# Kernel tuning notes

Measured on AMD Instinct MI355X. Metric: run time of the kernel, lower is better.

Reference implementation:

```python
import jax, jax.numpy as jnp
import numpy as np

H = 12          # num heads
D = 768         # hidden size
DH = D // H     # head dim = 64
DE = 768        # encoder hidden size


def setup_inputs() -> dict:
    key = jax.random.key(0)
    ks = jax.random.split(key, 10)
    s = 0.02
    return {
        "hidden_states": jax.random.normal(ks[0], (2, 2048, D), dtype=jnp.float32),
        "encoder_hidden_states": jax.random.normal(ks[1], (2, 4096, DE), dtype=jnp.float32),
        "Wq": jax.random.normal(ks[2], (D, D), dtype=jnp.float32) * s,
        "bq": jnp.zeros((D,), dtype=jnp.float32),
        "Wk": jax.random.normal(ks[3], (DE, D), dtype=jnp.float32) * s,
        "bk": jnp.zeros((D,), dtype=jnp.float32),
        "Wv": jax.random.normal(ks[4], (DE, D), dtype=jnp.float32) * s,
        "bv": jnp.zeros((D,), dtype=jnp.float32),
        "Wo": jax.random.normal(ks[5], (D, D), dtype=jnp.float32) * s,
        "bo": jnp.zeros((D,), dtype=jnp.float32),
    }


def _split_heads(x):
    # [B, S, D] -> [B, H, S, DH]
    B, S, _ = x.shape
    return x.reshape(B, S, H, DH).transpose(0, 2, 1, 3)


def reference(hidden_states, encoder_hidden_states, Wq, bq, Wk, bk, Wv, bv, Wo, bo):
    q = _split_heads(hidden_states @ Wq + bq)              # [B,H,Sq,DH]
    k = _split_heads(encoder_hidden_states @ Wk + bk)      # [B,H,Skv,DH]
    v = _split_heads(encoder_hidden_states @ Wv + bv)      # [B,H,Skv,DH]
    scale = 1.0 / jnp.sqrt(jnp.asarray(DH, dtype=q.dtype))
    scores = jnp.einsum("bhqd,bhkd->bhqk", q, k) * scale   # [B,H,Sq,Skv]
    probs = jax.nn.softmax(scores, axis=-1)
    ctx = jnp.einsum("bhqk,bhkd->bhqd", probs, v)          # [B,H,Sq,DH]
    B, _, Sq, _ = ctx.shape
    ctx = ctx.transpose(0, 2, 1, 3).reshape(B, Sq, D)      # [B,Sq,D]
    return ctx @ Wo + bo
```

## Files before the change

### kernel.cpp

```cpp
#include <hip/hip_runtime.h>

typedef __attribute__((ext_vector_type(8))) short bf16x8;
typedef __attribute__((ext_vector_type(4))) float f32x4;
typedef __attribute__((ext_vector_type(8))) unsigned short u16x8;
typedef __attribute__((ext_vector_type(4))) unsigned short u16x4;
typedef __attribute__((ext_vector_type(4))) int i32x4;

static constexpr int Bsz = 2, SQ = 2048, SKV = 4096, Dm = 768, NH = 12, DH = 64;

#define WAITV(N) asm volatile("s_waitcnt vmcnt(" #N ")" ::: "memory")
#define WAITL0() asm volatile("s_waitcnt lgkmcnt(0)" ::: "memory")

static __device__ __forceinline__ unsigned short f2bf(float f) {
  unsigned int u = __float_as_uint(f);
  u += 0x7fff + ((u >> 16) & 1);
  return (unsigned short)(u >> 16);
}

static __device__ __forceinline__ float fexp2(float x) {
#if __has_builtin(__builtin_amdgcn_exp2f)
  return __builtin_amdgcn_exp2f(x);
#else
  float r; asm("v_exp_f32 %0, %1" : "=v"(r) : "v"(x)); return r;
#endif
}

static __device__ __forceinline__ int cvtpk(float lo, float hi) {
  int r; asm("v_cvt_pk_bf16_f32 %0, %1, %2" : "=v"(r) : "v"(lo), "v"(hi));
  return r;
}

__global__ void cvt2_kernel(const float* __restrict__ a, const float* __restrict__ b,
                            unsigned short* __restrict__ out, int n1, int ntot) {
  int i = blockIdx.x * blockDim.x + threadIdx.x;
  if (i >= ntot) return;
  const float4* p = (i < n1) ? (reinterpret_cast<const float4*>(a) + (size_t)i * 2)
                             : (reinterpret_cast<const float4*>(b) + (size_t)(i - n1) * 2);
  float4 x = p[0], y = p[1];
  u16x8 o;
  o[0] = f2bf(x.x); o[1] = f2bf(x.y); o[2] = f2bf(x.z); o[3] = f2bf(x.w);
  o[4] = f2bf(y.x); o[5] = f2bf(y.y); o[6] = f2bf(y.z); o[7] = f2bf(y.w);
  *(reinterpret_cast<u16x8*>(out) + i) = o;
}

__global__ void wtrans4(const float* __restrict__ Wq, const float* __restrict__ Wk,
                        const float* __restrict__ Wv, const float* __restrict__ Wo,
                        unsigned short* __restrict__ oq, unsigned short* __restrict__ ok,
                        unsigned short* __restrict__ ov, unsigned short* __restrict__ oo) {
  __shared__ float t[32][33];
  const int z = blockIdx.z;
  const float* W = (z == 0) ? Wq : (z == 1) ? Wk : (z == 2) ? Wv : Wo;
  unsigned short* WT = (z == 0) ? oq : (z == 1) ? ok : (z == 2) ? ov : oo;
  int n0 = blockIdx.x * 32, k0 = blockIdx.y * 32;
  int tx = threadIdx.x, ty = threadIdx.y;
  #pragma unroll
  for (int i = 0; i < 4; ++i)
    t[ty * 4 + i][tx] = W[(size_t)(k0 + ty * 4 + i) * Dm + n0 + tx];
  __syncthreads();
  #pragma unroll
  for (int i = 0; i < 4; ++i)
    WT[(size_t)(n0 + ty * 4 + i) * Dm + k0 + tx] = f2bf(t[tx][ty * 4 + i]);
}

__global__ void vtrans(const unsigned short* __restrict__ vb, unsigned short* __restrict__ vtp) {
  __shared__ unsigned short t[64][65];
  const int kt = blockIdx.x, h = blockIdx.y, b = blockIdx.z;
  const int tid = threadIdx.x;
  const int kr = tid >> 2, dc = (tid & 3) * 16;
  const unsigned short* src = vb + ((size_t)(b * SKV + kt * 64 + kr)) * Dm + h * DH + dc;
  u16x8 a0 = *(const u16x8*)src, a1 = *(const u16x8*)(src + 8);
  #pragma unroll
  for (int j = 0; j < 8; ++j) { t[kr][dc + j] = a0[j]; t[kr][dc + 8 + j] = a1[j]; }
  __syncthreads();
  const int d = tid >> 2, p0 = (tid & 3) * 16;
  u16x8 o0, o1;
  #pragma unroll
  for (int j = 0; j < 16; ++j) {
    int pos = p0 + j;
    int pos5 = pos & 31;
    int kv5 = ((pos5 >> 3) & 3) * 4 + ((pos5 >> 2) & 1) * 16 + (pos5 & 3);
    int kv = (pos & 32) | kv5;
    unsigned short v = t[kv][d];
    if (j < 8) o0[j] = v; else o1[j - 8] = v;
  }
  unsigned short* dst = vtp + ((size_t)(b * NH + h) * DH + d) * SKV + kt * 64 + p0;
  *(u16x8*)dst = o0;
  *(u16x8*)(dst + 8) = o1;
}

template <int BM, int BN, bool F32OUT>
static __device__ __forceinline__ void gemm_body(const unsigned short* __restrict__ A,
                                                 const unsigned short* __restrict__ BT,
                                                 const float* __restrict__ bias,
                                                 void* __restrict__ Cout, float scale,
                                                 int row0, int col0,
                                                 unsigned short* As, unsigned short* Bs) {
  const int tid = threadIdx.x;
  const int wave = tid >> 6, lane = tid & 63;
  const int wr = wave >> 1, wc = wave & 1;
  const int lrow = lane & 15, lg = lane >> 4, lk8 = lg << 3;
  constexpr int MI = BM / 32, NJ = BN / 32;
  constexpr int AG = BM / 64, BG = BN / 64, LPS = AG + BG;
  constexpr int KS = Dm / 32;
  f32x4 acc[MI][NJ] = {};

  const unsigned short* ap[AG]; int ae[AG];
  const unsigned short* bp[BG]; int be[BG];
  #pragma unroll
  for (int j = 0; j < AG; ++j) {
    int e = (tid + j * 256) * 8; int r = e >> 5, c = e & 31;
    ap[j] = A + (size_t)(row0 + r) * Dm + c; ae[j] = e;
  }
  #pragma unroll
  for (int j = 0; j < BG; ++j) {
    int e = (tid + j * 256) * 8; int r = e >> 5, c = e & 31;
    bp[j] = BT + (size_t)(col0 + r) * Dm + c; be[j] = e;
  }

  auto stage = [&](int buf) {
    #pragma unroll
    for (int j = 0; j < AG; ++j) {
      __builtin_amdgcn_global_load_lds(
          (const __attribute__((address_space(1))) void*)ap[j],
          (__attribute__((address_space(3))) void*)(As + buf * (BM * 32) + ae[j]), 16, 0, 0);
      ap[j] += 32;
    }
    #pragma unroll
    for (int j = 0; j < BG; ++j) {
      __builtin_amdgcn_global_load_lds(
          (const __attribute__((address_space(1))) void*)bp[j],
          (__attribute__((address_space(3))) void*)(Bs + buf * (BN * 32) + be[j]), 16, 0, 0);
      bp[j] += 32;
    }
  };

  auto step = [&](int buf, bool doStage, bool last) {
    if (last) { WAITV(0); }
    else { if constexpr (LPS == 4) { WAITV(4); } else { WAITV(3); } }
    __builtin_amdgcn_s_barrier();
    bf16x8 a[MI], b[NJ];
    #pragma unroll
    for (int mi = 0; mi < MI; ++mi)
      a[mi] = *(const bf16x8*)&As[buf * (BM * 32) + (wr * (BM / 2) + mi * 16 + lrow) * 32 + lk8];
    #pragma unroll
    for (int nj = 0; nj < NJ; ++nj)
      b[nj] = *(const bf16x8*)&Bs[buf * (BN * 32) + (wc * (BN / 2) + nj * 16 + lrow) * 32 + lk8];
    WAITL0();
    __builtin_amdgcn_s_barrier();
    if (doStage) stage(buf);
    #pragma unroll
    for (int mi = 0; mi < MI; ++mi)
      #pragma unroll
      for (int nj = 0; nj < NJ; ++nj)
        acc[mi][nj] = __builtin_amdgcn_mfma_f32_16x16x32_bf16(b[nj], a[mi], acc[mi][nj], 0, 0, 0);
  };

  stage(0); stage(1);
  for (int ki = 0; ki + 2 < KS; ki += 2) { step(0, true, false); step(1, true, false); }
  step(0, false, false);
  step(1, false, true);

  #pragma unroll
  for (int mi = 0; mi < MI; ++mi) {
    const int grow = row0 + wr * (BM / 2) + mi * 16 + lrow;
    #pragma unroll
    for (int nj = 0; nj < NJ; ++nj) {
      const int gcolb = col0 + wc * (BN / 2) + nj * 16 + (lg << 2);
      const f32x4 bb = *(const f32x4*)&bias[gcolb];
      if constexpr (F32OUT) {
        f32x4 v;
        #pragma unroll
        for (int r = 0; r < 4; ++r) v[r] = (acc[mi][nj][r] + bb[r]) * scale;
        *(f32x4*)((float*)Cout + (size_t)grow * Dm + gcolb) = v;
      } else {
        u16x4 o;
        #pragma unroll
        for (int r = 0; r < 4; ++r) o[r] = f2bf((acc[mi][nj][r] + bb[r]) * scale);
        *(u16x4*)((unsigned short*)Cout + (size_t)grow * Dm + gcolb) = o;
      }
    }
  }
}

__global__ __launch_bounds__(256) void qkv_gemm(const unsigned short* __restrict__ hsb,
                                                const unsigned short* __restrict__ ehsb,
                                                const unsigned short* __restrict__ wqt,
                                                const unsigned short* __restrict__ wkt,
                                                const unsigned short* __restrict__ wvt,
                                                const float* __restrict__ bq,
                                                const float* __restrict__ bk,
                                                const float* __restrict__ bv,
                                                unsigned short* __restrict__ qb,
                                                unsigned short* __restrict__ kb,
                                                unsigned short* __restrict__ vb) {
  __shared__ unsigned short As[2 * 128 * 32];
  __shared__ unsigned short Bs[2 * 128 * 32];
  const int tile = blockIdx.y;
  const unsigned short *A, *BT; const float* bias; unsigned short* out;
  float scale; int row0;
  if (tile < 32)      { A = hsb;  BT = wqt; bias = bq; out = qb; scale = 0.18033688f; row0 = tile * 128; }
  else if (tile < 96) { A = ehsb; BT = wkt; bias = bk; out = kb; scale = 1.0f;        row0 = (tile - 32) * 128; }
  else                { A = ehsb; BT = wvt; bias = bv; out = vb; scale = 1.0f;        row0 = (tile - 96) * 128; }
  gemm_body<128, 128, false>(A, BT, bias, out, scale, row0, blockIdx.x * 128, As, Bs);
}

__global__ __launch_bounds__(256) void o_gemm(const unsigned short* __restrict__ A,
                                              const unsigned short* __restrict__ BT,
                                              const float* __restrict__ bias,
                                              float* __restrict__ Cout) {
  __shared__ unsigned short As[2 * 128 * 32];
  __shared__ unsigned short Bs[2 * 64 * 32];
  gemm_body<128, 64, true>(A, BT, bias, Cout, 1.0f, blockIdx.y * 128, blockIdx.x * 64, As, Bs);
}

__global__ __launch_bounds__(256) void attn_kernel(const unsigned short* __restrict__ Q,
                                                   const unsigned short* __restrict__ K,
                                                   const unsigned short* __restrict__ VT,
                                                   unsigned short* __restrict__ Ctx) {
  __shared__ unsigned short Ks[2][64 * 64];
  __shared__ unsigned short Vs[2][64 * 64];
  const int qt = blockIdx.x, h = blockIdx.y, b = blockIdx.z;
  const int tid = threadIdx.x;
  const int wave = tid >> 6, lane = tid & 63;
  const int lrow = lane & 15, lg = lane >> 4, lk8 = lg << 3;
  const size_t qoff = (size_t)b * SQ * Dm + (size_t)h * DH;
  const size_t koff = (size_t)b * SKV * Dm + (size_t)h * DH;
  const size_t voff = (size_t)(b * NH + h) * DH * SKV;

  const int qrow = qt * 64 + wave * 16 + lrow;
  const bf16x8 qa0 = *(const bf16x8*)(Q + qoff + (size_t)qrow * Dm + lk8);
  const bf16x8 qa1 = *(const bf16x8*)(Q + qoff + (size_t)qrow * Dm + 32 + lk8);

  bf16x8 ones;
  #pragma unroll
  for (int j = 0; j < 8; ++j) ones[j] = (short)0x3F80;

  const unsigned short *kp0, *kp1, *vp0, *vp1;
  int de0, de1;
  {
    int db0 = tid * 16, db1 = (tid + 256) * 16;
    int r0 = db0 >> 7, cb0 = db0 & 127, r1 = db1 >> 7, cb1 = db1 & 127;
    int sc0 = (cb0 ^ ((r0 & 7) << 4)) >> 1, sc1 = (cb1 ^ ((r1 & 7) << 4)) >> 1;
    kp0 = K + koff + (size_t)r0 * Dm + sc0;  kp1 = K + koff + (size_t)r1 * Dm + sc1;
    vp0 = VT + voff + (size_t)r0 * SKV + sc0; vp1 = VT + voff + (size_t)r1 * SKV + sc1;
    de0 = db0 >> 1; de1 = db1 >> 1;
  }

  auto stage = [&](int buf) {
    __builtin_amdgcn_global_load_lds((const __attribute__((address_space(1))) void*)kp0,
        (__attribute__((address_space(3))) void*)(&Ks[buf][de0]), 16, 0, 0);
    __builtin_amdgcn_global_load_lds((const __attribute__((address_space(1))) void*)vp0,
        (__attribute__((address_space(3))) void*)(&Vs[buf][de0]), 16, 0, 0);
    __builtin_amdgcn_global_load_lds((const __attribute__((address_space(1))) void*)kp1,
        (__attribute__((address_space(3))) void*)(&Ks[buf][de1]), 16, 0, 0);
    __builtin_amdgcn_global_load_lds((const __attribute__((address_space(1))) void*)vp1,
        (__attribute__((address_space(3))) void*)(&Vs[buf][de1]), 16, 0, 0);
    kp0 += 64 * Dm; kp1 += 64 * Dm; vp0 += 64; vp1 += 64;
  };

  f32x4 acc[4] = {};
  f32x4 acc_l = {};
  const int swz = (lrow & 7) << 4;

  auto tilebody = [&](int buf, bool doStage, bool last) {
    if (last) { WAITV(0); } else { WAITV(4); }
    __builtin_amdgcn_s_barrier();

    f32x4 s[4] = {};
    __builtin_amdgcn_s_setprio(1);
    #pragma unroll
    for (int ks = 0; ks < 2; ++ks)
      #pragma unroll
      for (int nj = 0; nj < 4; ++nj) {
        const int cb = (ks * 64 + lg * 16) ^ swz;
        bf16x8 kf = *(const bf16x8*)((const char*)&Ks[buf][0] + (nj * 16 + lrow) * 128 + cb);
        s[nj] = __builtin_amdgcn_mfma_f32_16x16x32_bf16(kf, ks ? qa1 : qa0, s[nj], 0, 0, 0);
      }
    __builtin_amdgcn_s_setprio(0);

    float e[4][4];
    #pragma unroll
    for (int nj = 0; nj < 4; ++nj)
      #pragma unroll
      for (int r = 0; r < 4; ++r) e[nj][r] = fexp2(s[nj][r]);

    #pragma unroll
    for (int ks = 0; ks < 2; ++ks) {
      i32x4 pw;
      pw[0] = cvtpk(e[2 * ks][0], e[2 * ks][1]);
      pw[1] = cvtpk(e[2 * ks][2], e[2 * ks][3]);
      pw[2] = cvtpk(e[2 * ks + 1][0], e[2 * ks + 1][1]);
      pw[3] = cvtpk(e[2 * ks + 1][2], e[2 * ks + 1][3]);
      bf16x8 pa = __builtin_bit_cast(bf16x8, pw);
      __builtin_amdgcn_s_setprio(1);
      #pragma unroll
      for (int dj = 0; dj < 4; ++dj) {
        const int cb = (ks * 64 + lg * 16) ^ swz;
        bf16x8 vf = *(const bf16x8*)((const char*)&Vs[buf][0] + (dj * 16 + lrow) * 128 + cb);
        acc[dj] = __builtin_amdgcn_mfma_f32_16x16x32_bf16(vf, pa, acc[dj], 0, 0, 0);
      }
      acc_l = __builtin_amdgcn_mfma_f32_16x16x32_bf16(ones, pa, acc_l, 0, 0, 0);
      __builtin_amdgcn_s_setprio(0);
    }

    WAITL0();
    __builtin_amdgcn_s_barrier();
    if (doStage) stage(buf);
  };

  stage(0); stage(1);
  constexpr int NT = SKV / 64;
  for (int t = 0; t + 2 < NT; t += 2) { tilebody(0, true, false); tilebody(1, true, false); }
  tilebody(0, false, false);
  tilebody(1, false, true);

  const float linv = 1.0f / acc_l[0];
  #pragma unroll
  for (int dj = 0; dj < 4; ++dj) {
    u16x4 o;
    #pragma unroll
    for (int r = 0; r < 4; ++r) o[r] = f2bf(acc[dj][r] * linv);
    *(u16x4*)(Ctx + qoff + (size_t)qrow * Dm + dj * 16 + (lg << 2)) = o;
  }
}

extern "C" void kernel_launch(void* const* d_in, const int* in_sizes, int n_in,
                              void* d_out, int out_size, void* d_ws, size_t ws_size,
                              hipStream_t stream) {
  const float* hs  = (const float*)d_in[0];
  const float* ehs = (const float*)d_in[1];
  const float* Wq  = (const float*)d_in[2];
  const float* bq  = (const float*)d_in[3];
  const float* Wk  = (const float*)d_in[4];
  const float* bk  = (const float*)d_in[5];
  const float* Wv  = (const float*)d_in[6];
  const float* bv  = (const float*)d_in[7];
  const float* Wo  = (const float*)d_in[8];
  const float* bo  = (const float*)d_in[9];
  float* out = (float*)d_out;

  unsigned short* hsb  = (unsigned short*)d_ws;
  unsigned short* ehsb = hsb  + (size_t)Bsz * SQ * Dm;
  unsigned short* wqt  = ehsb + (size_t)Bsz * SKV * Dm;
  unsigned short* wkt  = wqt + (size_t)Dm * Dm;
  unsigned short* wvt  = wkt + (size_t)Dm * Dm;
  unsigned short* wot  = wvt + (size_t)Dm * Dm;
  unsigned short* qb   = wot + (size_t)Dm * Dm;
  unsigned short* kb   = qb  + (size_t)Bsz * SQ * Dm;
  unsigned short* vb   = kb  + (size_t)Bsz * SKV * Dm;
  unsigned short* ctxb = vb  + (size_t)Bsz * SKV * Dm;
  unsigned short* vtp  = ehsb;

  const int nHS = Bsz * SQ * Dm, nEHS = Bsz * SKV * Dm;
  const int n1 = nHS / 8, ntot = (nHS + nEHS) / 8;
  cvt2_kernel<<<(ntot + 255) / 256, 256, 0, stream>>>(hs, ehs, hsb, n1, ntot);

  wtrans4<<<dim3(24, 24, 4), dim3(32, 8), 0, stream>>>(Wq, Wk, Wv, Wo, wqt, wkt, wvt, wot);

  qkv_gemm<<<dim3(6, 160), 256, 0, stream>>>(hsb, ehsb, wqt, wkt, wvt, bq, bk, bv, qb, kb, vb);

  vtrans<<<dim3(SKV / 64, NH, Bsz), 256, 0, stream>>>(vb, vtp);

  attn_kernel<<<dim3(SQ / 64, NH, Bsz), 256, 0, stream>>>(qb, kb, vtp, ctxb);

  o_gemm<<<dim3(12, 32), 256, 0, stream>>>(ctxb, wot, bo, out);
}
```

Baseline: 247.8 us.

## Triple-buffer GEMM and attention pipelines, two query strips per attention wave

Both the GEMM body and the attention kernel move from double to triple LDS buffering. The next tile is staged right after a single barrier instead of behind a second barrier and lgkmcnt wait. The attention kernel now runs 128 threads, where each wave covers 32 query rows (two 16-row strips), so every K/V fragment read from LDS feeds twice as many MFMAs. This cuts barriers per iteration and LDS traffic per FLOP, at the cost of more registers per wave and more LDS per block, which may lower occupancy.

```diff
diff --git a/kernel.cpp b/kernel.cpp
--- a/kernel.cpp
+++ b/kernel.cpp
@@ -9,7 +9,7 @@
 static constexpr int Bsz = 2, SQ = 2048, SKV = 4096, Dm = 768, NH = 12, DH = 64;
 
 #define WAITV(N) asm volatile("s_waitcnt vmcnt(" #N ")" ::: "memory")
-#define WAITL0() asm volatile("s_waitcnt lgkmcnt(0)" ::: "memory")
+#define BARRIER() asm volatile("s_barrier" ::: "memory")
 
 static __device__ __forceinline__ unsigned short f2bf(float f) {
   unsigned int u = __float_as_uint(f);
@@ -98,10 +98,9 @@
   const int tid = threadIdx.x;
   const int wave = tid >> 6, lane = tid & 63;
   const int wr = wave >> 1, wc = wave & 1;
-  const int lrow = lane & 15, lg = lane >> 4, lk8 = lg << 3;
+  const int lrow = lane & 15, lk8 = (lane >> 4) << 3;
   constexpr int MI = BM / 32, NJ = BN / 32;
   constexpr int AG = BM / 64, BG = BN / 64, LPS = AG + BG;
-  constexpr int KS = Dm / 32;
   f32x4 acc[MI][NJ] = {};
 
   const unsigned short* ap[AG]; int ae[AG];
@@ -134,10 +133,11 @@
     }
   };
 
-  auto step = [&](int buf, bool doStage, bool last) {
-    if (last) { WAITV(0); }
-    else { if constexpr (LPS == 4) { WAITV(4); } else { WAITV(3); } }
-    __builtin_amdgcn_s_barrier();
+  auto step = [&](int buf, int mode) {
+    if (mode < 2) { if constexpr (LPS == 4) { WAITV(4); } else { WAITV(3); } }
+    else          { WAITV(0); }
+    BARRIER();
+    if (mode == 0) stage(buf == 0 ? 2 : buf - 1);
     bf16x8 a[MI], b[NJ];
     #pragma unroll
     for (int mi = 0; mi < MI; ++mi)
@@ -145,9 +145,6 @@
     #pragma unroll
     for (int nj = 0; nj < NJ; ++nj)
       b[nj] = *(const bf16x8*)&Bs[buf * (BN * 32) + (wc * (BN / 2) + nj * 16 + lrow) * 32 + lk8];
-    WAITL0();
-    __builtin_amdgcn_s_barrier();
-    if (doStage) stage(buf);
     #pragma unroll
     for (int mi = 0; mi < MI; ++mi)
       #pragma unroll
@@ -156,16 +153,19 @@
   };
 
   stage(0); stage(1);
-  for (int ki = 0; ki + 2 < KS; ki += 2) { step(0, true, false); step(1, true, false); }
-  step(0, false, false);
-  step(1, false, true);
+  step(0, 0);
+  for (int base = 1; base <= 19; base += 3) {
+    step(1, 0); step(2, 0); step(0, 0);
+  }
+  step(1, 1);
+  step(2, 2);
 
   #pragma unroll
   for (int mi = 0; mi < MI; ++mi) {
     const int grow = row0 + wr * (BM / 2) + mi * 16 + lrow;
     #pragma unroll
     for (int nj = 0; nj < NJ; ++nj) {
-      const int gcolb = col0 + wc * (BN / 2) + nj * 16 + (lg << 2);
+      const int gcolb = col0 + wc * (BN / 2) + nj * 16 + ((lane >> 4) << 2);
       const f32x4 bb = *(const f32x4*)&bias[gcolb];
       if constexpr (F32OUT) {
         f32x4 v;
@@ -193,8 +193,8 @@
                                                 unsigned short* __restrict__ qb,
                                                 unsigned short* __restrict__ kb,
                                                 unsigned short* __restrict__ vb) {
-  __shared__ unsigned short As[2 * 128 * 32];
-  __shared__ unsigned short Bs[2 * 128 * 32];
+  __shared__ unsigned short As[3 * 128 * 32];
+  __shared__ unsigned short Bs[3 * 128 * 32];
   const int tile = blockIdx.y;
   const unsigned short *A, *BT; const float* bias; unsigned short* out;
   float scale; int row0;
@@ -208,17 +208,17 @@
                                               const unsigned short* __restrict__ BT,
                                               const float* __restrict__ bias,
                                               float* __restrict__ Cout) {
-  __shared__ unsigned short As[2 * 128 * 32];
-  __shared__ unsigned short Bs[2 * 64 * 32];
+  __shared__ unsigned short As[3 * 128 * 32];
+  __shared__ unsigned short Bs[3 * 64 * 32];
   gemm_body<128, 64, true>(A, BT, bias, Cout, 1.0f, blockIdx.y * 128, blockIdx.x * 64, As, Bs);
 }
 
-__global__ __launch_bounds__(256) void attn_kernel(const unsigned short* __restrict__ Q,
-                                                   const unsigned short* __restrict__ K,
-                                                   const unsigned short* __restrict__ VT,
-                                                   unsigned short* __restrict__ Ctx) {
-  __shared__ unsigned short Ks[2][64 * 64];
-  __shared__ unsigned short Vs[2][64 * 64];
+__global__ __launch_bounds__(128, 2) void attn_kernel(const unsigned short* __restrict__ Q,
+                                                      const unsigned short* __restrict__ K,
+                                                      const unsigned short* __restrict__ VT,
+                                                      unsigned short* __restrict__ Ctx) {
+  __shared__ unsigned short Ks[3][64 * 64];
+  __shared__ unsigned short Vs[3][64 * 64];
   const int qt = blockIdx.x, h = blockIdx.y, b = blockIdx.z;
   const int tid = threadIdx.x;
   const int wave = tid >> 6, lane = tid & 63;
@@ -227,100 +227,119 @@
   const size_t koff = (size_t)b * SKV * Dm + (size_t)h * DH;
   const size_t voff = (size_t)(b * NH + h) * DH * SKV;
 
-  const int qrow = qt * 64 + wave * 16 + lrow;
-  const bf16x8 qa0 = *(const bf16x8*)(Q + qoff + (size_t)qrow * Dm + lk8);
-  const bf16x8 qa1 = *(const bf16x8*)(Q + qoff + (size_t)qrow * Dm + 32 + lk8);
+  const int qrow0 = qt * 64 + wave * 32 + lrow;
+  const int qrow1 = qrow0 + 16;
+  const bf16x8 qa00 = *(const bf16x8*)(Q + qoff + (size_t)qrow0 * Dm + lk8);
+  const bf16x8 qa01 = *(const bf16x8*)(Q + qoff + (size_t)qrow0 * Dm + 32 + lk8);
+  const bf16x8 qa10 = *(const bf16x8*)(Q + qoff + (size_t)qrow1 * Dm + lk8);
+  const bf16x8 qa11 = *(const bf16x8*)(Q + qoff + (size_t)qrow1 * Dm + 32 + lk8);
 
   bf16x8 ones;
   #pragma unroll
   for (int j = 0; j < 8; ++j) ones[j] = (short)0x3F80;
 
-  const unsigned short *kp0, *kp1, *vp0, *vp1;
-  int de0, de1;
-  {
-    int db0 = tid * 16, db1 = (tid + 256) * 16;
-    int r0 = db0 >> 7, cb0 = db0 & 127, r1 = db1 >> 7, cb1 = db1 & 127;
-    int sc0 = (cb0 ^ ((r0 & 7) << 4)) >> 1, sc1 = (cb1 ^ ((r1 & 7) << 4)) >> 1;
-    kp0 = K + koff + (size_t)r0 * Dm + sc0;  kp1 = K + koff + (size_t)r1 * Dm + sc1;
-    vp0 = VT + voff + (size_t)r0 * SKV + sc0; vp1 = VT + voff + (size_t)r1 * SKV + sc1;
-    de0 = db0 >> 1; de1 = db1 >> 1;
+  const unsigned short* kp[4];
+  const unsigned short* vp[4];
+  int de[4];
+  #pragma unroll
+  for (int c = 0; c < 4; ++c) {
+    int db = (tid + c * 128) * 16;
+    int r = db >> 7, cb = db & 127;
+    int sc = (cb ^ ((r & 7) << 4)) >> 1;
+    kp[c] = K + koff + (size_t)r * Dm + sc;
+    vp[c] = VT + voff + (size_t)r * SKV + sc;
+    de[c] = db >> 1;
   }
 
   auto stage = [&](int buf) {
-    __builtin_amdgcn_global_load_lds((const __attribute__((address_space(1))) void*)kp0,
-        (__attribute__((address_space(3))) void*)(&Ks[buf][de0]), 16, 0, 0);
-    __builtin_amdgcn_global_load_lds((const __attribute__((address_space(1))) void*)vp0,
-        (__attribute__((address_space(3))) void*)(&Vs[buf][de0]), 16, 0, 0);
-    __builtin_amdgcn_global_load_lds((const __attribute__((address_space(1))) void*)kp1,
-        (__attribute__((address_space(3))) void*)(&Ks[buf][de1]), 16, 0, 0);
-    __builtin_amdgcn_global_load_lds((const __attribute__((address_space(1))) void*)vp1,
-        (__attribute__((address_space(3))) void*)(&Vs[buf][de1]), 16, 0, 0);
-    kp0 += 64 * Dm; kp1 += 64 * Dm; vp0 += 64; vp1 += 64;
+    #pragma unroll
+    for (int c = 0; c < 4; ++c) {
+      __builtin_amdgcn_global_load_lds((const __attribute__((address_space(1))) void*)kp[c],
+          (__attribute__((address_space(3))) void*)(&Ks[buf][de[c]]), 16, 0, 0);
+      __builtin_amdgcn_global_load_lds((const __attribute__((address_space(1))) void*)vp[c],
+          (__attribute__((address_space(3))) void*)(&Vs[buf][de[c]]), 16, 0, 0);
+      kp[c] += 64 * Dm; vp[c] += 64;
+    }
   };
 
-  f32x4 acc[4] = {};
-  f32x4 acc_l = {};
+  f32x4 acc0[4] = {}, acc1[4] = {};
+  f32x4 accl0 = {}, accl1 = {};
   const int swz = (lrow & 7) << 4;
 
-  auto tilebody = [&](int buf, bool doStage, bool last) {
-    if (last) { WAITV(0); } else { WAITV(4); }
-    __builtin_amdgcn_s_barrier();
-
-    f32x4 s[4] = {};
+  auto body = [&](int buf, int mode) {
+    if (mode < 2) { WAITV(8); } else { WAITV(0); }
+    BARRIER();
+    if (mode == 0) stage(buf == 0 ? 2 : buf - 1);
+
+    f32x4 s0[4] = {}, s1[4] = {};
     __builtin_amdgcn_s_setprio(1);
     #pragma unroll
-    for (int ks = 0; ks < 2; ++ks)
+    for (int ks = 0; ks < 2; ++ks) {
+      bf16x8 kf[4];
       #pragma unroll
       for (int nj = 0; nj < 4; ++nj) {
         const int cb = (ks * 64 + lg * 16) ^ swz;
-        bf16x8 kf = *(const bf16x8*)((const char*)&Ks[buf][0] + (nj * 16 + lrow) * 128 + cb);
-        s[nj] = __builtin_amdgcn_mfma_f32_16x16x32_bf16(kf, ks ? qa1 : qa0, s[nj], 0, 0, 0);
+        kf[nj] = *(const bf16x8*)((const char*)&Ks[buf][0] + (nj * 16 + lrow) * 128 + cb);
       }
+      #pragma unroll
+      for (int nj = 0; nj < 4; ++nj) {
+        s0[nj] = __builtin_amdgcn_mfma_f32_16x16x32_bf16(kf[nj], ks ? qa01 : qa00, s0[nj], 0, 0, 0);
+        s1[nj] = __builtin_amdgcn_mfma_f32_16x16x32_bf16(kf[nj], ks ? qa11 : qa10, s1[nj], 0, 0, 0);
+      }
+    }
     __builtin_amdgcn_s_setprio(0);
 
-    float e[4][4];
+    float e0[4][4], e1[4][4];
     #pragma unroll
     for (int nj = 0; nj < 4; ++nj)
       #pragma unroll
-      for (int r = 0; r < 4; ++r) e[nj][r] = fexp2(s[nj][r]);
+      for (int r = 0; r < 4; ++r) { e0[nj][r] = fexp2(s0[nj][r]); e1[nj][r] = fexp2(s1[nj][r]); }
 
     #pragma unroll
     for (int ks = 0; ks < 2; ++ks) {
-      i32x4 pw;
-      pw[0] = cvtpk(e[2 * ks][0], e[2 * ks][1]);
-      pw[1] = cvtpk(e[2 * ks][2], e[2 * ks][3]);
-      pw[2] = cvtpk(e[2 * ks + 1][0], e[2 * ks + 1][1]);
-      pw[3] = cvtpk(e[2 * ks + 1][2], e[2 * ks + 1][3]);
-      bf16x8 pa = __builtin_bit_cast(bf16x8, pw);
+      i32x4 pw0, pw1;
+      pw0[0] = cvtpk(e0[2 * ks][0], e0[2 * ks][1]);
+      pw0[1] = cvtpk(e0[2 * ks][2], e0[2 * ks][3]);
+      pw0[2] = cvtpk(e0[2 * ks + 1][0], e0[2 * ks + 1][1]);
+      pw0[3] = cvtpk(e0[2 * ks + 1][2], e0[2 * ks + 1][3]);
+      pw1[0] = cvtpk(e1[2 * ks][0], e1[2 * ks][1]);
+      pw1[1] = cvtpk(e1[2 * ks][2], e1[2 * ks][3]);
+      pw1[2] = cvtpk(e1[2 * ks + 1][0], e1[2 * ks + 1][1]);
+      pw1[3] = cvtpk(e1[2 * ks + 1][2], e1[2 * ks + 1][3]);
+      bf16x8 pa0 = __builtin_bit_cast(bf16x8, pw0);
+      bf16x8 pa1 = __builtin_bit_cast(bf16x8, pw1);
       __builtin_amdgcn_s_setprio(1);
       #pragma unroll
       for (int dj = 0; dj < 4; ++dj) {
         const int cb = (ks * 64 + lg * 16) ^ swz;
         bf16x8 vf = *(const bf16x8*)((const char*)&Vs[buf][0] + (dj * 16 + lrow) * 128 + cb);
-        acc[dj] = __builtin_amdgcn_mfma_f32_16x16x32_bf16(vf, pa, acc[dj], 0, 0, 0);
+        acc0[dj] = __builtin_amdgcn_mfma_f32_16x16x32_bf16(vf, pa0, acc0[dj], 0, 0, 0);
+        acc1[dj] = __builtin_amdgcn_mfma_f32_16x16x32_bf16(vf, pa1, acc1[dj], 0, 0, 0);
       }
-      acc_l = __builtin_amdgcn_mfma_f32_16x16x32_bf16(ones, pa, acc_l, 0, 0, 0);
+      accl0 = __builtin_amdgcn_mfma_f32_16x16x32_bf16(ones, pa0, accl0, 0, 0, 0);
+      accl1 = __builtin_amdgcn_mfma_f32_16x16x32_bf16(ones, pa1, accl1, 0, 0, 0);
       __builtin_amdgcn_s_setprio(0);
     }
-
-    WAITL0();
-    __builtin_amdgcn_s_barrier();
-    if (doStage) stage(buf);
   };
 
   stage(0); stage(1);
-  constexpr int NT = SKV / 64;
-  for (int t = 0; t + 2 < NT; t += 2) { tilebody(0, true, false); tilebody(1, true, false); }
-  tilebody(0, false, false);
-  tilebody(1, false, true);
-
-  const float linv = 1.0f / acc_l[0];
+  body(0, 0);
+  for (int base = 1; base <= 58; base += 3) {
+    body(1, 0); body(2, 0); body(0, 0);
+  }
+  body(1, 0);
+  body(2, 1);
+  body(0, 2);
+
+  const float li0 = 1.0f / accl0[0];
+  const float li1 = 1.0f / accl1[0];
   #pragma unroll
   for (int dj = 0; dj < 4; ++dj) {
-    u16x4 o;
-    #pragma unroll
-    for (int r = 0; r < 4; ++r) o[r] = f2bf(acc[dj][r] * linv);
-    *(u16x4*)(Ctx + qoff + (size_t)qrow * Dm + dj * 16 + (lg << 2)) = o;
+    u16x4 o0, o1;
+    #pragma unroll
+    for (int r = 0; r < 4; ++r) { o0[r] = f2bf(acc0[dj][r] * li0); o1[r] = f2bf(acc1[dj][r] * li1); }
+    *(u16x4*)(Ctx + qoff + (size_t)qrow0 * Dm + dj * 16 + (lg << 2)) = o0;
+    *(u16x4*)(Ctx + qoff + (size_t)qrow1 * Dm + dj * 16 + (lg << 2)) = o1;
   }
 }
 
@@ -361,7 +380,7 @@
 
   vtrans<<<dim3(SKV / 64, NH, Bsz), 256, 0, stream>>>(vb, vtp);
 
-  attn_kernel<<<dim3(SQ / 64, NH, Bsz), 256, 0, stream>>>(qb, kb, vtp, ctxb);
+  attn_kernel<<<dim3(SQ / 64, NH, Bsz), 128, 0, stream>>>(qb, kb, vtp, ctxb);
 
   o_gemm<<<dim3(12, 32), 256, 0, stream>>>(ctxb, wot, bo, out);
 }
```

Measured after the change: 248.0 us. Within noise of the previous version (+0.1%).
